# Kernel tuning notes

Measured on AMD Instinct MI355X. Metric: run time of the kernel, lower is better.

Reference implementation:

```python
import jax, jax.numpy as jnp
import numpy as np

FEATHER = (16, 16)          # in_feather_size
OUT_FEATHER = (16, 16)      # out_feather_size
F = FEATHER[0] * FEATHER[1]            # 256
INNER = (F + 1) ** 2                   # 66049
OUT = OUT_FEATHER[0] * OUT_FEATHER[1]  # 256
B = 2048


def setup_inputs() -> dict:
    key = jax.random.key(0)
    kx, kw, kb = jax.random.split(key, 3)
    x = jax.random.normal(kx, (B, F), dtype=jnp.float32)
    # nn.Linear(INNER, OUT): weight [OUT, INNER], bias [OUT]
    bound = 1.0 / np.sqrt(INNER)
    W = jax.random.uniform(kw, (OUT, INNER), dtype=jnp.float32, minval=-bound, maxval=bound)
    b = jax.random.uniform(kb, (OUT,), dtype=jnp.float32, minval=-bound, maxval=bound)
    return {"x": x, "W": W, "b": b}


def reference(x, W, b):
    # x: [B, F] -> prepend 1 -> x1: [B, F+1]
    x = x.reshape(-1, F)
    ones = jnp.ones((x.shape[0], 1), dtype=x.dtype)
    x1 = jnp.concatenate([ones, x], axis=-1)          # [B, F+1]
    # batched outer product, flattened: [B, (F+1)^2]
    outer = (x1[:, :, None] * x1[:, None, :]).reshape(x.shape[0], INNER)
    y = outer @ W.T + b                               # [B, OUT]
    return y.reshape(-1, OUT_FEATHER[0], OUT_FEATHER[1])
```

## Files before the change

### kernel.cpp

```cpp
#include <hip/hip_runtime.h>
#include <cstdint>
#include <cstddef>


typedef _Float16 half8 __attribute__((ext_vector_type(8)));
typedef float    f32x4 __attribute__((ext_vector_type(4)));

#define LD8(p) (*(const half8*)(p))
#define WAITVM(N) asm volatile("s_waitcnt vmcnt(" #N ")" ::: "memory")
#define WAITLGKM  asm volatile("s_waitcnt lgkmcnt(0)" ::: "memory")

__device__ __forceinline__ void gload_lds16(const void* g, void* lds) {
  __builtin_amdgcn_global_load_lds(
      (const __attribute__((address_space(1))) uint32_t*)g,
      (__attribute__((address_space(3))) uint32_t*)lds, 16, 0, 0);
}

__global__ void conv_w_k(const float* __restrict__ W, _Float16* __restrict__ Wp) {
  int t  = blockIdx.x * 256 + threadIdx.x;
  int l  = t & 63;
  int f  = (t >> 6) & 15;
  int jc = (t >> 10) & 7;
  int ii = t >> 13;
  int o  = f * 16 + (l & 15);
  int j0 = jc * 32 + (l >> 4) * 8;
  half8 h;
  if (ii < 257) {
    const float* src = W + (size_t)o * 66049 + (size_t)ii * 257 + j0;
#pragma unroll
    for (int e = 0; e < 8; ++e) h[e] = (_Float16)src[e];
  } else {
    const float* src = W + (size_t)o * 66049 + 256;
#pragma unroll
    for (int e = 0; e < 8; ++e) h[e] = (_Float16)src[(size_t)(j0 + e) * 257];
  }
  *(half8*)(Wp + (size_t)t * 8) = h;
}

__global__ void conv_x1_k(const float* __restrict__ x, _Float16* __restrict__ X1g) {
  int t  = blockIdx.x * 256 + threadIdx.x;
  int j8 = t % 33;
  int b  = t / 33;
  half8 h;
#pragma unroll
  for (int u = 0; u < 8; ++u) {
    int jj = j8 * 8 + u;
    float v = (jj == 0) ? 1.0f : (jj <= 256 ? x[(size_t)b * 256 + (jj - 1)] : 0.0f);
    h[u] = (_Float16)v;
  }
  *(half8*)(X1g + (size_t)b * 264 + j8 * 8) = h;
}

__global__ void init_out_k(const float* __restrict__ x, const float* __restrict__ W,
                           const float* __restrict__ bias, float* __restrict__ Y) {
  int o = threadIdx.x;
  int b = blockIdx.x;
  float xl = x[(size_t)b * 256 + 255];
  float w  = W[(size_t)o * 66049 + 66048];
  Y[(size_t)b * 256 + o] = bias[o] + xl * xl * w;
}

__global__ __launch_bounds__(512, 4)
void gemm_k(const _Float16* __restrict__ Wp, const _Float16* __restrict__ X1g,
            float* __restrict__ Y) {
  __shared__ __align__(16) _Float16 wbuf[4 * 8192];
  __shared__ _Float16 scal[9 * 128];

  const int bid = blockIdx.x;
  const int s   = bid & 31;
  const int mt  = bid >> 5;
  const int nii = (s < 2) ? 9 : 8;
  const int ii0 = s * 8 + (s < 2 ? s : 2);

  const int tid = threadIdx.x;
  const int l   = tid & 63;
  const int w   = tid >> 6;
  const int wm  = w >> 2;
  const int wn  = w & 3;
  const int ln  = l & 15;
  const int ks  = l >> 4;

  for (int t = tid; t < nii * 128; t += 512) {
    int k = t >> 7, m = t & 127;
    int ii = ii0 + k; if (ii > 256) ii = 256;
    scal[k * 128 + m] = X1g[(size_t)(mt * 128 + m) * 264 + ii];
  }

  const _Float16* xr = X1g + (size_t)(mt * 128 + wm * 64 + ln) * 264 + ks * 8;

  const char* gW   = (const char*)Wp + (size_t)ii0 * 131072 + w * 1024 + l * 16;
  char*       ldsW = (char*)wbuf + w * 1024;

  const int nsteps = nii * 8;

  gload_lds16(gW +     0, ldsW);            gload_lds16(gW +  8192, ldsW + 8192);
  gload_lds16(gW + 131072, ldsW + 16384);   gload_lds16(gW + 139264, ldsW + 24576);
  gload_lds16(gW + 262144, ldsW + 32768);   gload_lds16(gW + 270336, ldsW + 40960);
  WAITVM(4);
  WAITLGKM;
  __builtin_amdgcn_s_barrier();

  f32x4 acc[4][4];
#pragma unroll
  for (int mf = 0; mf < 4; ++mf)
#pragma unroll
    for (int nf = 0; nf < 4; ++nf) acc[mf][nf] = (f32x4){0.f, 0.f, 0.f, 0.f};

  int st  = 0;
  int sk  = 3, sjc = 0;
  for (int jc = 0; jc < 8; ++jc) {
    half8 cur[4];
#pragma unroll
    for (int mf = 0; mf < 4; ++mf)
      cur[mf] = LD8(xr + (size_t)(mf * 16) * 264 + jc * 32);

    for (int k = 0; k < nii; ++k, ++st) {
      if (st + 3 < nsteps) {
        const int blk = (sk * 8 + sjc) * 16384;
        char* d = ldsW + ((st + 3) & 3) * 16384;
        gload_lds16(gW + blk, d);
        gload_lds16(gW + blk + 8192, d + 8192);
        ++sk; if (sk == nii) { sk = 0; ++sjc; }
      }

      _Float16 sv0 = scal[k * 128 + wm * 64 +  0 + ln];
      _Float16 sv1 = scal[k * 128 + wm * 64 + 16 + ln];
      _Float16 sv2 = scal[k * 128 + wm * 64 + 32 + ln];
      _Float16 sv3 = scal[k * 128 + wm * 64 + 48 + ln];

      const _Float16* wb = wbuf + (st & 3) * 8192 + (wn * 4) * 512 + l * 8;
      half8 bf0 = LD8(wb);
      half8 bf1 = LD8(wb + 512);
      half8 bf2 = LD8(wb + 1024);
      half8 bf3 = LD8(wb + 1536);

      __builtin_amdgcn_s_setprio(1);
      {
        half8 v0 = {sv0, sv0, sv0, sv0, sv0, sv0, sv0, sv0};
        half8 af = cur[0] * v0;
        acc[0][0] = __builtin_amdgcn_mfma_f32_16x16x32_f16(af, bf0, acc[0][0], 0, 0, 0);
        acc[0][1] = __builtin_amdgcn_mfma_f32_16x16x32_f16(af, bf1, acc[0][1], 0, 0, 0);
        acc[0][2] = __builtin_amdgcn_mfma_f32_16x16x32_f16(af, bf2, acc[0][2], 0, 0, 0);
        acc[0][3] = __builtin_amdgcn_mfma_f32_16x16x32_f16(af, bf3, acc[0][3], 0, 0, 0);
      }
      {
        half8 v1 = {sv1, sv1, sv1, sv1, sv1, sv1, sv1, sv1};
        half8 af = cur[1] * v1;
        acc[1][0] = __builtin_amdgcn_mfma_f32_16x16x32_f16(af, bf0, acc[1][0], 0, 0, 0);
        acc[1][1] = __builtin_amdgcn_mfma_f32_16x16x32_f16(af, bf1, acc[1][1], 0, 0, 0);
        acc[1][2] = __builtin_amdgcn_mfma_f32_16x16x32_f16(af, bf2, acc[1][2], 0, 0, 0);
        acc[1][3] = __builtin_amdgcn_mfma_f32_16x16x32_f16(af, bf3, acc[1][3], 0, 0, 0);
      }
      {
        half8 v2 = {sv2, sv2, sv2, sv2, sv2, sv2, sv2, sv2};
        half8 af = cur[2] * v2;
        acc[2][0] = __builtin_amdgcn_mfma_f32_16x16x32_f16(af, bf0, acc[2][0], 0, 0, 0);
        acc[2][1] = __builtin_amdgcn_mfma_f32_16x16x32_f16(af, bf1, acc[2][1], 0, 0, 0);
        acc[2][2] = __builtin_amdgcn_mfma_f32_16x16x32_f16(af, bf2, acc[2][2], 0, 0, 0);
        acc[2][3] = __builtin_amdgcn_mfma_f32_16x16x32_f16(af, bf3, acc[2][3], 0, 0, 0);
      }
      {
        half8 v3 = {sv3, sv3, sv3, sv3, sv3, sv3, sv3, sv3};
        half8 af = cur[3] * v3;
        acc[3][0] = __builtin_amdgcn_mfma_f32_16x16x32_f16(af, bf0, acc[3][0], 0, 0, 0);
        acc[3][1] = __builtin_amdgcn_mfma_f32_16x16x32_f16(af, bf1, acc[3][1], 0, 0, 0);
        acc[3][2] = __builtin_amdgcn_mfma_f32_16x16x32_f16(af, bf2, acc[3][2], 0, 0, 0);
        acc[3][3] = __builtin_amdgcn_mfma_f32_16x16x32_f16(af, bf3, acc[3][3], 0, 0, 0);
      }
      __builtin_amdgcn_s_setprio(0);

      if (st < nsteps - 1) {
        if (st <= nsteps - 4)      { WAITVM(4); }
        else if (st == nsteps - 3) { WAITVM(2); }
        else                       { WAITVM(0); }
        __builtin_amdgcn_s_barrier();
      }
    }
  }

  float* yb = Y + (size_t)(mt * 128 + wm * 64) * 256 + wn * 64;
  const int r0 = ks * 4;
#pragma unroll
  for (int mf = 0; mf < 4; ++mf)
#pragma unroll
    for (int nf = 0; nf < 4; ++nf)
#pragma unroll
      for (int r = 0; r < 4; ++r)
        unsafeAtomicAdd(&yb[(size_t)(mf * 16 + r0 + r) * 256 + nf * 16 + ln],
                        acc[mf][nf][r]);
}

__global__ void fb_k(const float* __restrict__ x, const float* __restrict__ W,
                     const float* __restrict__ bias, float* __restrict__ Y) {
  __shared__ float x1[257];
  int b = blockIdx.x, o = threadIdx.x;
  x1[o + 1] = x[(size_t)b * 256 + o];
  if (o == 0) x1[0] = 1.0f;
  __syncthreads();
  const float* Wr = W + (size_t)o * 66049;
  float acc = bias[o];
  for (int i = 0; i < 257; ++i) {
    const float* wr = Wr + (size_t)i * 257;
    float p = 0.f;
    for (int j = 0; j < 257; ++j) p = fmaf(x1[j], wr[j], p);
    acc = fmaf(x1[i], p, acc);
  }
  Y[(size_t)b * 256 + o] = acc;
}

extern "C" void kernel_launch(void* const* d_in, const int* in_sizes, int n_in,
                              void* d_out, int out_size, void* d_ws, size_t ws_size,
                              hipStream_t stream) {
  const float* x = (const float*)d_in[0];
  const float* W = (const float*)d_in[1];
  const float* b = (const float*)d_in[2];
  float* y = (float*)d_out;

  const size_t WPB = (size_t)258 * 8 * 16 * 64 * 16;
  const size_t X1B = (size_t)2048 * 264 * 2;
  if (ws_size < WPB + X1B) {
    fb_k<<<2048, 256, 0, stream>>>(x, W, b, y);
    return;
  }
  _Float16* Wp  = (_Float16*)d_ws;
  _Float16* X1g = (_Float16*)((char*)d_ws + WPB);

  conv_w_k<<<8256, 256, 0, stream>>>(W, Wp);
  conv_x1_k<<<264, 256, 0, stream>>>(x, X1g);
  init_out_k<<<2048, 256, 0, stream>>>(x, W, b, y);
  gemm_k<<<512, 512, 0, stream>>>(Wp, X1g, y);
}
```

Before: 145.9 us.

## Restructure GEMM pipeline with paired k-steps, 8-slot LDS ring and register scalars

Rewrites the main GEMM loop to process two k-steps per barrier, using an 8-slot LDS ring buffer with deeper prefetch. The per-row scale factors now sit in registers instead of an LDS table, and the ii split is rebalanced so the last slice handles 9 rows plus a zero-padded tenth. The next jc's x fragments are also prefetched early. Each block uses twice the shared memory, so launch bounds drop from 4 to 2 blocks per SM, trading occupancy for fewer barriers and more latency hiding.

```diff
diff --git a/kernel.cpp b/kernel.cpp
--- a/kernel.cpp
+++ b/kernel.cpp
@@ -8,13 +8,14 @@
 
 #define LD8(p) (*(const half8*)(p))
 #define WAITVM(N) asm volatile("s_waitcnt vmcnt(" #N ")" ::: "memory")
-#define WAITLGKM  asm volatile("s_waitcnt lgkmcnt(0)" ::: "memory")
 
 __device__ __forceinline__ void gload_lds16(const void* g, void* lds) {
   __builtin_amdgcn_global_load_lds(
       (const __attribute__((address_space(1))) uint32_t*)g,
       (__attribute__((address_space(3))) uint32_t*)lds, 16, 0, 0);
 }
+
+#define MFMA(a, b, c) __builtin_amdgcn_mfma_f32_16x16x32_f16((a), (b), (c), 0, 0, 0)
 
 __global__ void conv_w_k(const float* __restrict__ W, _Float16* __restrict__ Wp) {
   int t  = blockIdx.x * 256 + threadIdx.x;
@@ -60,17 +61,113 @@
   Y[(size_t)b * 256 + o] = bias[o] + xl * xl * w;
 }
 
-__global__ __launch_bounds__(512, 4)
+template<int NII>
+__device__ __forceinline__ void core_fn(
+    const char* __restrict__ gW,
+    char* __restrict__ ldsW,
+    const _Float16* __restrict__ wbuf,
+    const _Float16* __restrict__ xr,
+    half8 s80, half8 s81, half8 s82, half8 s83,
+    _Float16 s90, _Float16 s91, _Float16 s92, _Float16 s93,
+    int wn, int l, f32x4 acc[4][4])
+{
+  constexpr int NP = NII / 2;
+  half8 cur[4], curN[4];
+#pragma unroll
+  for (int mf = 0; mf < 4; ++mf)
+    cur[mf] = LD8(xr + (size_t)(mf * 16) * 264);
+
+#pragma unroll
+  for (int k0 = 0; k0 < 6; ++k0) {
+    char* d = ldsW + k0 * 16384;
+    gload_lds16(gW + (size_t)k0 * 131072, d);
+    gload_lds16(gW + (size_t)k0 * 131072 + 8192, d + 8192);
+  }
+
+  for (int jc = 0; jc < 8; ++jc) {
+#pragma unroll
+    for (int kp = 0; kp < NP; ++kp) {
+      const int k  = 2 * kp;
+      const int p  = jc * NP + kp;
+      const int st = 2 * p;
+
+      if (jc < 7) { WAITVM(8); }
+      else {
+        if (kp <= NP - 3)      { WAITVM(8); }
+        else if (kp == NP - 2) { WAITVM(4); }
+        else                   { WAITVM(0); }
+      }
+      __builtin_amdgcn_s_barrier();
+
+      const _Float16* wb0 = wbuf + (size_t)((st    ) & 7) * 8192 + wn * 2048 + l * 8;
+      const _Float16* wb1 = wbuf + (size_t)((st + 1) & 7) * 8192 + wn * 2048 + l * 8;
+      half8 a0 = LD8(wb0), a1 = LD8(wb0 + 512), a2 = LD8(wb0 + 1024), a3 = LD8(wb0 + 1536);
+      half8 b0 = LD8(wb1), b1 = LD8(wb1 + 512), b2 = LD8(wb1 + 1024), b3 = LD8(wb1 + 1536);
+
+      if (kp == NP - 2 && jc < 7) {
+#pragma unroll
+        for (int mf = 0; mf < 4; ++mf)
+          curN[mf] = LD8(xr + (size_t)(mf * 16) * 264 + (jc + 1) * 32);
+      }
+
+      if (p + 3 <= 8 * NP - 1) {
+        const int pt  = p + 3;
+        const int jct = pt / NP;
+        const int ktp = pt - jct * NP;
+        const size_t boff = (size_t)(ktp * 16 + jct) * 16384;
+        const int sl = (2 * pt) & 7;
+        char* d0 = ldsW + sl * 16384;
+        gload_lds16(gW + boff, d0);
+        gload_lds16(gW + boff + 8192, d0 + 8192);
+        char* d1 = d0 + 16384;
+        gload_lds16(gW + boff + 131072, d1);
+        gload_lds16(gW + boff + 131072 + 8192, d1 + 8192);
+      }
+
+      __builtin_amdgcn_s_setprio(1);
+#pragma unroll
+      for (int mf = 0; mf < 4; ++mf) {
+        _Float16 e = (k < 8)
+            ? ((mf == 0) ? s80[k] : (mf == 1) ? s81[k] : (mf == 2) ? s82[k] : s83[k])
+            : ((mf == 0) ? s90 : (mf == 1) ? s91 : (mf == 2) ? s92 : s93);
+        half8 v = {e, e, e, e, e, e, e, e};
+        half8 af = cur[mf] * v;
+        acc[mf][0] = MFMA(af, a0, acc[mf][0]);
+        acc[mf][1] = MFMA(af, a1, acc[mf][1]);
+        acc[mf][2] = MFMA(af, a2, acc[mf][2]);
+        acc[mf][3] = MFMA(af, a3, acc[mf][3]);
+      }
+#pragma unroll
+      for (int mf = 0; mf < 4; ++mf) {
+        const int k1 = k + 1;
+        _Float16 e = (k1 < 8)
+            ? ((mf == 0) ? s80[k1] : (mf == 1) ? s81[k1] : (mf == 2) ? s82[k1] : s83[k1])
+            : ((mf == 0) ? s90 : (mf == 1) ? s91 : (mf == 2) ? s92 : s93);
+        half8 v = {e, e, e, e, e, e, e, e};
+        half8 af = cur[mf] * v;
+        acc[mf][0] = MFMA(af, b0, acc[mf][0]);
+        acc[mf][1] = MFMA(af, b1, acc[mf][1]);
+        acc[mf][2] = MFMA(af, b2, acc[mf][2]);
+        acc[mf][3] = MFMA(af, b3, acc[mf][3]);
+      }
+      __builtin_amdgcn_s_setprio(0);
+    }
+    if (jc < 7) {
+#pragma unroll
+      for (int mf = 0; mf < 4; ++mf) cur[mf] = curN[mf];
+    }
+  }
+}
+
+__global__ __launch_bounds__(512, 2)
 void gemm_k(const _Float16* __restrict__ Wp, const _Float16* __restrict__ X1g,
             float* __restrict__ Y) {
-  __shared__ __align__(16) _Float16 wbuf[4 * 8192];
-  __shared__ _Float16 scal[9 * 128];
+  __shared__ __align__(16) _Float16 wbuf[8 * 8192];
 
   const int bid = blockIdx.x;
   const int s   = bid & 31;
   const int mt  = bid >> 5;
-  const int nii = (s < 2) ? 9 : 8;
-  const int ii0 = s * 8 + (s < 2 ? s : 2);
+  const int ii0 = s * 8;
 
   const int tid = threadIdx.x;
   const int l   = tid & 63;
@@ -80,103 +177,35 @@
   const int ln  = l & 15;
   const int ks  = l >> 4;
 
-  for (int t = tid; t < nii * 128; t += 512) {
-    int k = t >> 7, m = t & 127;
-    int ii = ii0 + k; if (ii > 256) ii = 256;
-    scal[k * 128 + m] = X1g[(size_t)(mt * 128 + m) * 264 + ii];
-  }
-
-  const _Float16* xr = X1g + (size_t)(mt * 128 + wm * 64 + ln) * 264 + ks * 8;
+  const int row = mt * 128 + wm * 64 + ln;
+  const _Float16* xr = X1g + (size_t)row * 264 + ks * 8;
+
+  half8 s80 = LD8(X1g + (size_t)(row +  0) * 264 + ii0);
+  half8 s81 = LD8(X1g + (size_t)(row + 16) * 264 + ii0);
+  half8 s82 = LD8(X1g + (size_t)(row + 32) * 264 + ii0);
+  half8 s83 = LD8(X1g + (size_t)(row + 48) * 264 + ii0);
+  _Float16 s90 = (_Float16)0.f, s91 = (_Float16)0.f,
+           s92 = (_Float16)0.f, s93 = (_Float16)0.f;
+  if (s == 31) {
+    s90 = X1g[(size_t)(row +  0) * 264 + 256];
+    s91 = X1g[(size_t)(row + 16) * 264 + 256];
+    s92 = X1g[(size_t)(row + 32) * 264 + 256];
+    s93 = X1g[(size_t)(row + 48) * 264 + 256];
+  }
 
   const char* gW   = (const char*)Wp + (size_t)ii0 * 131072 + w * 1024 + l * 16;
   char*       ldsW = (char*)wbuf + w * 1024;
 
-  const int nsteps = nii * 8;
-
-  gload_lds16(gW +     0, ldsW);            gload_lds16(gW +  8192, ldsW + 8192);
-  gload_lds16(gW + 131072, ldsW + 16384);   gload_lds16(gW + 139264, ldsW + 24576);
-  gload_lds16(gW + 262144, ldsW + 32768);   gload_lds16(gW + 270336, ldsW + 40960);
-  WAITVM(4);
-  WAITLGKM;
-  __builtin_amdgcn_s_barrier();
-
   f32x4 acc[4][4];
 #pragma unroll
   for (int mf = 0; mf < 4; ++mf)
 #pragma unroll
     for (int nf = 0; nf < 4; ++nf) acc[mf][nf] = (f32x4){0.f, 0.f, 0.f, 0.f};
 
-  int st  = 0;
-  int sk  = 3, sjc = 0;
-  for (int jc = 0; jc < 8; ++jc) {
-    half8 cur[4];
-#pragma unroll
-    for (int mf = 0; mf < 4; ++mf)
-      cur[mf] = LD8(xr + (size_t)(mf * 16) * 264 + jc * 32);
-
-    for (int k = 0; k < nii; ++k, ++st) {
-      if (st + 3 < nsteps) {
-        const int blk = (sk * 8 + sjc) * 16384;
-        char* d = ldsW + ((st + 3) & 3) * 16384;
-        gload_lds16(gW + blk, d);
-        gload_lds16(gW + blk + 8192, d + 8192);
-        ++sk; if (sk == nii) { sk = 0; ++sjc; }
-      }
-
-      _Float16 sv0 = scal[k * 128 + wm * 64 +  0 + ln];
-      _Float16 sv1 = scal[k * 128 + wm * 64 + 16 + ln];
-      _Float16 sv2 = scal[k * 128 + wm * 64 + 32 + ln];
-      _Float16 sv3 = scal[k * 128 + wm * 64 + 48 + ln];
-
-      const _Float16* wb = wbuf + (st & 3) * 8192 + (wn * 4) * 512 + l * 8;
-      half8 bf0 = LD8(wb);
-      half8 bf1 = LD8(wb + 512);
-      half8 bf2 = LD8(wb + 1024);
-      half8 bf3 = LD8(wb + 1536);
-
-      __builtin_amdgcn_s_setprio(1);
-      {
-        half8 v0 = {sv0, sv0, sv0, sv0, sv0, sv0, sv0, sv0};
-        half8 af = cur[0] * v0;
-        acc[0][0] = __builtin_amdgcn_mfma_f32_16x16x32_f16(af, bf0, acc[0][0], 0, 0, 0);
-        acc[0][1] = __builtin_amdgcn_mfma_f32_16x16x32_f16(af, bf1, acc[0][1], 0, 0, 0);
-        acc[0][2] = __builtin_amdgcn_mfma_f32_16x16x32_f16(af, bf2, acc[0][2], 0, 0, 0);
-        acc[0][3] = __builtin_amdgcn_mfma_f32_16x16x32_f16(af, bf3, acc[0][3], 0, 0, 0);
-      }
-      {
-        half8 v1 = {sv1, sv1, sv1, sv1, sv1, sv1, sv1, sv1};
-        half8 af = cur[1] * v1;
-        acc[1][0] = __builtin_amdgcn_mfma_f32_16x16x32_f16(af, bf0, acc[1][0], 0, 0, 0);
-        acc[1][1] = __builtin_amdgcn_mfma_f32_16x16x32_f16(af, bf1, acc[1][1], 0, 0, 0);
-        acc[1][2] = __builtin_amdgcn_mfma_f32_16x16x32_f16(af, bf2, acc[1][2], 0, 0, 0);
-        acc[1][3] = __builtin_amdgcn_mfma_f32_16x16x32_f16(af, bf3, acc[1][3], 0, 0, 0);
-      }
-      {
-        half8 v2 = {sv2, sv2, sv2, sv2, sv2, sv2, sv2, sv2};
-        half8 af = cur[2] * v2;
-        acc[2][0] = __builtin_amdgcn_mfma_f32_16x16x32_f16(af, bf0, acc[2][0], 0, 0, 0);
-        acc[2][1] = __builtin_amdgcn_mfma_f32_16x16x32_f16(af, bf1, acc[2][1], 0, 0, 0);
-        acc[2][2] = __builtin_amdgcn_mfma_f32_16x16x32_f16(af, bf2, acc[2][2], 0, 0, 0);
-        acc[2][3] = __builtin_amdgcn_mfma_f32_16x16x32_f16(af, bf3, acc[2][3], 0, 0, 0);
-      }
-      {
-        half8 v3 = {sv3, sv3, sv3, sv3, sv3, sv3, sv3, sv3};
-        half8 af = cur[3] * v3;
-        acc[3][0] = __builtin_amdgcn_mfma_f32_16x16x32_f16(af, bf0, acc[3][0], 0, 0, 0);
-        acc[3][1] = __builtin_amdgcn_mfma_f32_16x16x32_f16(af, bf1, acc[3][1], 0, 0, 0);
-        acc[3][2] = __builtin_amdgcn_mfma_f32_16x16x32_f16(af, bf2, acc[3][2], 0, 0, 0);
-        acc[3][3] = __builtin_amdgcn_mfma_f32_16x16x32_f16(af, bf3, acc[3][3], 0, 0, 0);
-      }
-      __builtin_amdgcn_s_setprio(0);
-
-      if (st < nsteps - 1) {
-        if (st <= nsteps - 4)      { WAITVM(4); }
-        else if (st == nsteps - 3) { WAITVM(2); }
-        else                       { WAITVM(0); }
-        __builtin_amdgcn_s_barrier();
-      }
-    }
-  }
+  if (s == 31)
+    core_fn<10>(gW, ldsW, wbuf, xr, s80, s81, s82, s83, s90, s91, s92, s93, wn, l, acc);
+  else
+    core_fn<8>(gW, ldsW, wbuf, xr, s80, s81, s82, s83, s90, s91, s92, s93, wn, l, acc);
 
   float* yb = Y + (size_t)(mt * 128 + wm * 64) * 256 + wn * 64;
   const int r0 = ks * 4;
```

Measured after the change: 378.7 us. 160% more time.
